# Optimization experiments

Hardware: AMD Instinct MI355X
Metric: run time of the kernel (lower is better)

Reference implementation:

```python
import jax, jax.numpy as jnp
import numpy as np

BSZ, SEQLEN, NUM_TAGS = 64, 512, 48
START_TAG_ID, END_TAG_ID = 46, 47
EPS = 1e-12


def setup_inputs() -> dict:
    key = jax.random.key(0)
    k1, k2 = jax.random.split(key)
    transition = jax.random.normal(k1, (BSZ, SEQLEN, NUM_TAGS, NUM_TAGS), dtype=jnp.float32)
    target = jax.random.randint(k2, (BSZ, SEQLEN), 0, 46, dtype=jnp.int64)
    return {"transition": transition, "target": target}


def reference(transition, target):
    # transition: [B, S, T, T] float; target: [B, S] int
    B, S, T, _ = transition.shape

    # ---- gold path score (vectorized gather over time) ----
    prev = jnp.concatenate(
        [jnp.full((B, 1), START_TAG_ID, dtype=target.dtype), target[:, :-1]], axis=1
    )  # tag at t-1 (START at t=0)
    b = jnp.arange(B)[:, None]
    s = jnp.arange(S)[None, :]
    target_score = transition[b, s, prev, target].sum(axis=1)  # [B]

    # ---- log partition via forward algorithm (scan over time) ----
    trans_tm = jnp.moveaxis(transition, 1, 0)  # [S, B, T, T] time-major
    forw0 = trans_tm[0, :, START_TAG_ID, :]  # [B, T]

    def step(forw, tr_t):
        # tr_t: [B, T, T]; tmp[b, i, j] = forw[b, i] + tr_t[b, i, j]
        tmp = forw[:, :, None] + tr_t
        m = tmp.max(axis=1)  # [B, T]
        forw = jnp.log(jnp.exp(tmp - m[:, None, :]).sum(axis=1) + EPS) + m
        return forw, None

    forw, _ = jax.lax.scan(step, forw0, trans_tm[1:])
    loss = -target_score + forw[:, END_TAG_ID]  # [B]
    return loss.mean()  # reduction='mean'
```

## Files before the change

kernel.cpp:

```cpp
#include <hip/hip_runtime.h>
#include <hip/hip_bf16.h>


#define B_N 64
#define S_N 512
#define T_N 48
#define TT_N 2304
#define START_TAG 46
#define END_TAG 47
#define CHUNK_L 16
#define CPB 32
#define N_CHUNKS 2048
#define LN2F 0.6931471805599453f

typedef __bf16 bf16x4 __attribute__((ext_vector_type(4)));
typedef short short4v __attribute__((ext_vector_type(4)));
typedef float f32x4 __attribute__((ext_vector_type(4)));

static __device__ __forceinline__ f32x4 mfma16(bf16x4 a, bf16x4 b, f32x4 c) {
#if __has_builtin(__builtin_amdgcn_mfma_f32_16x16x16bf16_1k)
  return __builtin_amdgcn_mfma_f32_16x16x16bf16_1k(
      __builtin_bit_cast(short4v, a), __builtin_bit_cast(short4v, b), c, 0, 0, 0);
#else
  f32x4 d;
  asm("v_mfma_f32_16x16x16_bf16 %0, %1, %2, %3"
      : "=v"(d) : "v"(a), "v"(b), "v"(c));
  return d;
#endif
}

__global__ __launch_bounds__(256, 2) void crf_k1(const float* __restrict__ tr,
                                                 __bf16* __restrict__ wsH) {
  const int w = threadIdx.x >> 6, lane = threadIdx.x & 63;
  const int col = lane & 15, quad = lane >> 4;
  const int g = blockIdx.x * 4 + w;
  const float* __restrict__ base = tr + (size_t)g * (CHUNK_L * TT_N);

  bf16x4 bfr[3][3];
#pragma unroll
  for (int kb = 0; kb < 3; ++kb)
#pragma unroll
    for (int nt = 0; nt < 3; ++nt) {
      const float4 v = *(const float4*)(base + (size_t)((nt * 16 + col) * T_N + kb * 16 + quad * 4));
      bfr[kb][nt][0] = (__bf16)__expf(v.x);
      bfr[kb][nt][1] = (__bf16)__expf(v.y);
      bfr[kb][nt][2] = (__bf16)__expf(v.z);
      bfr[kb][nt][3] = (__bf16)__expf(v.w);
    }

  float st[3][3][4];
  {
    const float* nb = base + TT_N;
#pragma unroll
    for (int mt = 0; mt < 3; ++mt)
#pragma unroll
      for (int kt = 0; kt < 3; ++kt)
#pragma unroll
        for (int j = 0; j < 4; ++j)
          st[mt][kt][j] = nb[(kt * 16 + quad * 4 + j) * T_N + mt * 16 + col];
  }

  f32x4 acc[3][3];
  for (int t = 1; t < CHUNK_L; ++t) {
    bf16x4 a[3][3];
#pragma unroll
    for (int mt = 0; mt < 3; ++mt)
#pragma unroll
      for (int kt = 0; kt < 3; ++kt)
#pragma unroll
        for (int j = 0; j < 4; ++j)
          a[mt][kt][j] = (__bf16)__expf(st[mt][kt][j]);

    if (t < CHUNK_L - 1) {
      const float* nb = base + (size_t)(t + 1) * TT_N;
#pragma unroll
      for (int mt = 0; mt < 3; ++mt)
#pragma unroll
        for (int kt = 0; kt < 3; ++kt)
#pragma unroll
          for (int j = 0; j < 4; ++j)
            st[mt][kt][j] = nb[(kt * 16 + quad * 4 + j) * T_N + mt * 16 + col];
    }

#pragma unroll
    for (int mt = 0; mt < 3; ++mt)
#pragma unroll
      for (int nt = 0; nt < 3; ++nt) {
        f32x4 c = {0.f, 0.f, 0.f, 0.f};
        c = mfma16(a[mt][0], bfr[0][nt], c);
        c = mfma16(a[mt][1], bfr[1][nt], c);
        c = mfma16(a[mt][2], bfr[2][nt], c);
        acc[mt][nt] = c;
      }
#pragma unroll
    for (int mt = 0; mt < 3; ++mt)
#pragma unroll
      for (int nt = 0; nt < 3; ++nt)
#pragma unroll
        for (int r = 0; r < 4; ++r)
          bfr[mt][nt][r] = (__bf16)(acc[mt][nt][r] * 0.0078125f);
  }

  __bf16* out = wsH + (size_t)g * TT_N;
#pragma unroll
  for (int kb = 0; kb < 3; ++kb)
#pragma unroll
    for (int nt = 0; nt < 3; ++nt)
#pragma unroll
      for (int j = 0; j < 4; ++j)
        out[(kb * 16 + quad * 4 + j) * T_N + nt * 16 + col] = bfr[kb][nt][j];
}

#define LDS_RS 52
__global__ __launch_bounds__(256, 2) void crf_k2(const float* __restrict__ tr,
                                                 const int* __restrict__ tgt,
                                                 const __bf16* __restrict__ wsH,
                                                 float* __restrict__ wsLoss) {
  const int b = blockIdx.x;
  const int tid = threadIdx.x;
  const int w = tid >> 6, lane = tid & 63;
  const int col = lane & 15, quad = lane >> 4;

  __shared__ __align__(16) __bf16 Sl[3][T_N * LDS_RS];
  __shared__ float red[4];

  float ts = 0.f;
  for (int s = tid; s < S_N; s += 256) {
    const int tg = tgt[b * S_N + s];
    const int pv = (s == 0) ? START_TAG : tgt[b * S_N + s - 1];
    ts += tr[(size_t)(b * S_N + s) * TT_N + pv * T_N + tg];
  }
#pragma unroll
  for (int s2 = 1; s2 < 64; s2 <<= 1) ts += __shfl_xor(ts, s2);
  if (lane == 0) red[w] = ts;

  const __bf16* hb = wsH + (size_t)(b * CPB + w * 8) * TT_N;
  bf16x4 bfr[3][3];
#pragma unroll
  for (int kb = 0; kb < 3; ++kb)
#pragma unroll
    for (int nt = 0; nt < 3; ++nt)
#pragma unroll
      for (int j = 0; j < 4; ++j)
        bfr[kb][nt][j] = hb[(kb * 16 + quad * 4 + j) * T_N + nt * 16 + col];

  f32x4 acc[3][3];
  for (int c = 1; c < 8; ++c) {
    const __bf16* hc = hb + (size_t)c * TT_N;
    bf16x4 a[3][3];
#pragma unroll
    for (int mt = 0; mt < 3; ++mt)
#pragma unroll
      for (int kt = 0; kt < 3; ++kt)
        a[mt][kt] = *(const bf16x4*)(hc + (mt * 16 + col) * T_N + kt * 16 + quad * 4);
#pragma unroll
    for (int mt = 0; mt < 3; ++mt)
#pragma unroll
      for (int nt = 0; nt < 3; ++nt) {
        f32x4 c4 = {0.f, 0.f, 0.f, 0.f};
        c4 = mfma16(a[mt][0], bfr[0][nt], c4);
        c4 = mfma16(a[mt][1], bfr[1][nt], c4);
        c4 = mfma16(a[mt][2], bfr[2][nt], c4);
        acc[mt][nt] = c4;
      }
#pragma unroll
    for (int mt = 0; mt < 3; ++mt)
#pragma unroll
      for (int nt = 0; nt < 3; ++nt)
#pragma unroll
        for (int r = 0; r < 4; ++r)
          bfr[mt][nt][r] = (__bf16)(acc[mt][nt][r] * 32.0f);
  }

  if (w > 0) {
    __bf16* dst = &Sl[w - 1][0];
#pragma unroll
    for (int kb = 0; kb < 3; ++kb)
#pragma unroll
      for (int nt = 0; nt < 3; ++nt)
#pragma unroll
        for (int j = 0; j < 4; ++j)
          dst[(kb * 16 + quad * 4 + j) * LDS_RS + nt * 16 + col] = bfr[kb][nt][j];
  }
  __syncthreads();

  if (w == 0) {
    for (int m = 0; m < 3; ++m) {
      const __bf16* src = &Sl[m][0];
      bf16x4 a[3][3];
#pragma unroll
      for (int mt = 0; mt < 3; ++mt)
#pragma unroll
        for (int kt = 0; kt < 3; ++kt)
          a[mt][kt] = *(const bf16x4*)(src + (mt * 16 + col) * LDS_RS + kt * 16 + quad * 4);
#pragma unroll
      for (int mt = 0; mt < 3; ++mt)
#pragma unroll
        for (int nt = 0; nt < 3; ++nt) {
          f32x4 c4 = {0.f, 0.f, 0.f, 0.f};
          c4 = mfma16(a[mt][0], bfr[0][nt], c4);
          c4 = mfma16(a[mt][1], bfr[1][nt], c4);
          c4 = mfma16(a[mt][2], bfr[2][nt], c4);
          acc[mt][nt] = c4;
        }
#pragma unroll
      for (int mt = 0; mt < 3; ++mt)
#pragma unroll
        for (int nt = 0; nt < 3; ++nt)
#pragma unroll
          for (int r = 0; r < 4; ++r)
            bfr[mt][nt][r] = (__bf16)(acc[mt][nt][r] * 32.0f);
    }
    const float vv = __shfl(acc[2][2][3] * 32.0f, 62);
    if (lane == 0) {
      const float tsum = red[0] + red[1] + red[2] + red[3];
      const float logZ = logf(vv) + (float)(CPB * 105 - 31 * 5) * LN2F;
      wsLoss[b] = -tsum + logZ;
    }
  }
}

__global__ void crf_k3(const float* __restrict__ wsLoss, float* __restrict__ out) {
  float x = wsLoss[threadIdx.x];
#pragma unroll
  for (int s = 1; s < 64; s <<= 1) x += __shfl_xor(x, s);
  if (threadIdx.x == 0) out[0] = x * (1.0f / 64.0f);
}

extern "C" void kernel_launch(void* const* d_in, const int* in_sizes, int n_in,
                              void* d_out, int out_size, void* d_ws, size_t ws_size,
                              hipStream_t stream) {
  const float* tr = (const float*)d_in[0];
  const int* tgt = (const int*)d_in[1];
  __bf16* wsH = (__bf16*)d_ws;
  float* wsLoss = (float*)((char*)d_ws + (size_t)N_CHUNKS * TT_N * sizeof(__bf16));

  crf_k1<<<N_CHUNKS / 4, 256, 0, stream>>>(tr, wsH);
  crf_k2<<<B_N, 256, 0, stream>>>(tr, tgt, wsH, wsLoss);
  crf_k3<<<1, 64, 0, stream>>>(wsLoss, (float*)d_out);
}
```

Baseline: 410.6 us.

## Reverse chunk product order to enable vectorized row loads and stores

The chunk matrix product in the first kernel now runs backward in time, starting from an identity matrix. This lets each step load the transition matrix with contiguous float4 reads instead of strided scalar reads, and lets the result be written back with vector bf16x4 stores. Scaling moves from a per-step multiply into an exp bias subtracted before exponentiation. The cost is one extra MFMA step (16 instead of 15), and the change of product order and bias scaling has to stay numerically consistent with the fixed log-scale constant in the second kernel.

```diff
diff --git a/kernel.cpp b/kernel.cpp
--- a/kernel.cpp
+++ b/kernel.cpp
@@ -12,6 +12,7 @@
 #define CPB 32
 #define N_CHUNKS 2048
 #define LN2F 0.6931471805599453f
+#define EXP_BIAS 4.852030263919617f
 
 typedef __bf16 bf16x4 __attribute__((ext_vector_type(4)));
 typedef short short4v __attribute__((ext_vector_type(4)));
@@ -40,46 +41,40 @@
 #pragma unroll
   for (int kb = 0; kb < 3; ++kb)
 #pragma unroll
-    for (int nt = 0; nt < 3; ++nt) {
-      const float4 v = *(const float4*)(base + (size_t)((nt * 16 + col) * T_N + kb * 16 + quad * 4));
-      bfr[kb][nt][0] = (__bf16)__expf(v.x);
-      bfr[kb][nt][1] = (__bf16)__expf(v.y);
-      bfr[kb][nt][2] = (__bf16)__expf(v.z);
-      bfr[kb][nt][3] = (__bf16)__expf(v.w);
-    }
-
-  float st[3][3][4];
+    for (int nt = 0; nt < 3; ++nt)
+#pragma unroll
+      for (int j = 0; j < 4; ++j)
+        bfr[kb][nt][j] = (kb == nt && (quad * 4 + j) == col) ? (__bf16)1.0f : (__bf16)0.0f;
+
+  f32x4 st[3][3];
   {
-    const float* nb = base + TT_N;
+    const float* nb = base + 15 * TT_N;
 #pragma unroll
     for (int mt = 0; mt < 3; ++mt)
 #pragma unroll
       for (int kt = 0; kt < 3; ++kt)
+        st[mt][kt] = *(const f32x4*)(nb + (size_t)((mt * 16 + col) * T_N + kt * 16 + quad * 4));
+  }
+
+  f32x4 acc[3][3];
+  for (int t = CHUNK_L - 1; t >= 0; --t) {
+    const float bias = (t == CHUNK_L - 1) ? 0.0f : EXP_BIAS;
+    bf16x4 a[3][3];
+#pragma unroll
+    for (int mt = 0; mt < 3; ++mt)
+#pragma unroll
+      for (int kt = 0; kt < 3; ++kt)
 #pragma unroll
         for (int j = 0; j < 4; ++j)
-          st[mt][kt][j] = nb[(kt * 16 + quad * 4 + j) * T_N + mt * 16 + col];
-  }
-
-  f32x4 acc[3][3];
-  for (int t = 1; t < CHUNK_L; ++t) {
-    bf16x4 a[3][3];
-#pragma unroll
-    for (int mt = 0; mt < 3; ++mt)
-#pragma unroll
-      for (int kt = 0; kt < 3; ++kt)
-#pragma unroll
-        for (int j = 0; j < 4; ++j)
-          a[mt][kt][j] = (__bf16)__expf(st[mt][kt][j]);
-
-    if (t < CHUNK_L - 1) {
-      const float* nb = base + (size_t)(t + 1) * TT_N;
+          a[mt][kt][j] = (__bf16)__expf(st[mt][kt][j] - bias);
+
+    if (t > 0) {
+      const float* nb = base + (size_t)(t - 1) * TT_N;
 #pragma unroll
       for (int mt = 0; mt < 3; ++mt)
 #pragma unroll
         for (int kt = 0; kt < 3; ++kt)
-#pragma unroll
-          for (int j = 0; j < 4; ++j)
-            st[mt][kt][j] = nb[(kt * 16 + quad * 4 + j) * T_N + mt * 16 + col];
+          st[mt][kt] = *(const f32x4*)(nb + (size_t)((mt * 16 + col) * T_N + kt * 16 + quad * 4));
     }
 
 #pragma unroll
@@ -98,7 +93,7 @@
       for (int nt = 0; nt < 3; ++nt)
 #pragma unroll
         for (int r = 0; r < 4; ++r)
-          bfr[mt][nt][r] = (__bf16)(acc[mt][nt][r] * 0.0078125f);
+          bfr[mt][nt][r] = (__bf16)acc[mt][nt][r];
   }
 
   __bf16* out = wsH + (size_t)g * TT_N;
@@ -106,9 +101,7 @@
   for (int kb = 0; kb < 3; ++kb)
 #pragma unroll
     for (int nt = 0; nt < 3; ++nt)
-#pragma unroll
-      for (int j = 0; j < 4; ++j)
-        out[(kb * 16 + quad * 4 + j) * T_N + nt * 16 + col] = bfr[kb][nt][j];
+      *(bf16x4*)(out + (size_t)((nt * 16 + col) * T_N + kb * 16 + quad * 4)) = bfr[kb][nt];
 }
 
 #define LDS_RS 52
```

Measured after the change: 412.0 us. Within noise of the previous version (+0.3%).
